# Optimization experiments

Hardware: AMD Instinct MI355X
Metric: run time of the kernel (lower is better)

## Reference

```python
import jax, jax.numpy as jnp
import numpy as np

D_MODEL = 2048
NUM_HEADS = 16
HEAD_DIM = D_MODEL // NUM_HEADS
D_FF = 4 * D_MODEL
B, L = 2, 2048
LN_EPS = 1e-6


def layer_norm(x, scale, bias):
    x32 = x.astype(jnp.float32)
    mu = jnp.mean(x32, axis=-1, keepdims=True)
    var = jnp.mean(jnp.square(x32 - mu), axis=-1, keepdims=True)
    return (x32 - mu) * jax.lax.rsqrt(var + LN_EPS) * scale + bias


def setup_inputs() -> dict:
    key = jax.random.key(0)
    ks = jax.random.split(key, 10)
    s = 1.0 / np.sqrt(D_MODEL)
    x = jax.random.normal(ks[0], (B, L, D_MODEL), dtype=jnp.float32)
    mask = jnp.tril(jnp.ones((L, L), dtype=bool))[None, None, :, :]  # causal [1,1,L,L]
    wq = jax.random.normal(ks[1], (D_MODEL, D_MODEL), jnp.float32) * s
    wk = jax.random.normal(ks[2], (D_MODEL, D_MODEL), jnp.float32) * s
    wv = jax.random.normal(ks[3], (D_MODEL, D_MODEL), jnp.float32) * s
    wo = jax.random.normal(ks[4], (D_MODEL, D_MODEL), jnp.float32) * s
    w1 = jax.random.normal(ks[5], (D_MODEL, D_FF), jnp.float32) * s
    b1 = jnp.zeros((D_FF,), jnp.float32)
    w2 = jax.random.normal(ks[6], (D_FF, D_MODEL), jnp.float32) * (1.0 / np.sqrt(D_FF))
    b2 = jnp.zeros((D_MODEL,), jnp.float32)
    ln1_scale = jnp.ones((D_MODEL,), jnp.float32)
    ln1_bias = jnp.zeros((D_MODEL,), jnp.float32)
    ln2_scale = jnp.ones((D_MODEL,), jnp.float32)
    ln2_bias = jnp.zeros((D_MODEL,), jnp.float32)
    return {"x": x, "mask": mask, "ln1_scale": ln1_scale, "ln1_bias": ln1_bias,
            "wq": wq, "wk": wk, "wv": wv, "wo": wo,
            "ln2_scale": ln2_scale, "ln2_bias": ln2_bias,
            "w1": w1, "b1": b1, "w2": w2, "b2": b2}


def reference(x, mask, ln1_scale, ln1_bias, wq, wk, wv, wo,
              ln2_scale, ln2_bias, w1, b1, w2, b2):
    residual = x
    h = layer_norm(x, ln1_scale, ln1_bias)
    b, l, _ = h.shape
    q = (h @ wq).reshape(b, l, NUM_HEADS, HEAD_DIM)
    k = (h @ wk).reshape(b, l, NUM_HEADS, HEAD_DIM)
    v = (h @ wv).reshape(b, l, NUM_HEADS, HEAD_DIM)
    scores = jnp.einsum('bqhd,bkhd->bhqk', q, k) / jnp.sqrt(jnp.float32(HEAD_DIM))
    scores = jnp.where(mask, scores, -100000.0)
    attn = jax.nn.softmax(scores, axis=-1)
    attn_out = jnp.einsum('bhqk,bkhd->bqhd', attn, v).reshape(b, l, D_MODEL)
    x = residual + attn_out @ wo
    mlp = jax.nn.gelu(layer_norm(x, ln2_scale, ln2_bias) @ w1 + b1)
    return x + mlp @ w2 + b2
```

## Files before the change

### kernel.cpp

```cpp
#include <hip/hip_runtime.h>
#include <hip/hip_bf16.h>

typedef unsigned short u16;
typedef __bf16 bf16x8 __attribute__((ext_vector_type(8)));
typedef float f32x4 __attribute__((ext_vector_type(4)));

#define D_MODEL 2048
#define D_FF    8192
#define NH      16
#define HD      128
#define BATCH   2
#define SEQ     2048
#define ROWS    (BATCH*SEQ)

__device__ __forceinline__ u16 f2bf(float f) {
  union { __hip_bfloat16 h; u16 u; } cv;
  cv.h = __float2bfloat16(f);
  return cv.u;
}

__device__ __forceinline__ void gload16(const u16* g, u16* l) {
  __builtin_amdgcn_global_load_lds((const __attribute__((address_space(1))) void*)g,
                                   (__attribute__((address_space(3))) void*)l,
                                   16, 0, 0);
}

__device__ __forceinline__ float gelu_f(float x) {
  const float k0 = 0.7978845608028654f, k1 = 0.044715f;
  return 0.5f * x * (1.0f + tanhf(k0 * (x + k1 * x * x * x)));
}

__global__ __launch_bounds__(256) void ln_bf16_kernel(
    const float* __restrict__ x, const float* __restrict__ sc,
    const float* __restrict__ bs, u16* __restrict__ out)
{
  __shared__ float red[8];
  const int row = blockIdx.x, t = threadIdx.x;
  const int w = t >> 6, l = t & 63;
  const float* xr = x + (size_t)row * D_MODEL;
  float4 a = ((const float4*)xr)[t*2];
  float4 b = ((const float4*)xr)[t*2+1];
  float s  = a.x+a.y+a.z+a.w + b.x+b.y+b.z+b.w;
  float s2 = a.x*a.x+a.y*a.y+a.z*a.z+a.w*a.w + b.x*b.x+b.y*b.y+b.z*b.z+b.w*b.w;
  for (int off = 32; off; off >>= 1) { s += __shfl_down(s, off); s2 += __shfl_down(s2, off); }
  if (l == 0) { red[w] = s; red[4+w] = s2; }
  __syncthreads();
  s  = red[0]+red[1]+red[2]+red[3];
  s2 = red[4]+red[5]+red[6]+red[7];
  const float mu  = s * (1.0f / D_MODEL);
  const float var = s2 * (1.0f / D_MODEL) - mu * mu;
  const float inv = rsqrtf(var + 1e-6f);
  float4 g0 = ((const float4*)sc)[t*2], g1 = ((const float4*)sc)[t*2+1];
  float4 q0 = ((const float4*)bs)[t*2], q1 = ((const float4*)bs)[t*2+1];
  union { u16 u[8]; uint4 v; } o;
  o.u[0] = f2bf((a.x-mu)*inv*g0.x + q0.x);
  o.u[1] = f2bf((a.y-mu)*inv*g0.y + q0.y);
  o.u[2] = f2bf((a.z-mu)*inv*g0.z + q0.z);
  o.u[3] = f2bf((a.w-mu)*inv*g0.w + q0.w);
  o.u[4] = f2bf((b.x-mu)*inv*g1.x + q1.x);
  o.u[5] = f2bf((b.y-mu)*inv*g1.y + q1.y);
  o.u[6] = f2bf((b.z-mu)*inv*g1.z + q1.z);
  o.u[7] = f2bf((b.w-mu)*inv*g1.w + q1.w);
  *(uint4*)(&out[(size_t)row * D_MODEL + t*8]) = o.v;
}

__global__ __launch_bounds__(256) void transpose_w(
    const float* __restrict__ in, u16* __restrict__ out, int R, int C)
{
  __shared__ float tile[32][33];
  const int t = threadIdx.x;
  const int c0 = blockIdx.x*32, r0 = blockIdx.y*32;
  const int col = t & 31, rb = t >> 5;
#pragma unroll
  for (int i = 0; i < 4; ++i)
    tile[rb + i*8][col] = in[(size_t)(r0 + rb + i*8)*C + c0 + col];
  __syncthreads();
#pragma unroll
  for (int i = 0; i < 4; ++i)
    out[(size_t)(c0 + rb + i*8)*R + r0 + col] = f2bf(tile[col][rb + i*8]);
}

__global__ __launch_bounds__(256) void transpose_v(
    const u16* __restrict__ qkv, u16* __restrict__ vt)
{
  __shared__ u16 tile[32][34];
  const int t = threadIdx.x;
  const int b = blockIdx.z;
  const int c0 = blockIdx.x*32, r0 = blockIdx.y*32;
  const int col = t & 31, rb = t >> 5;
  const u16* inb = qkv + (size_t)b*SEQ*3*D_MODEL + 2*D_MODEL;
#pragma unroll
  for (int i = 0; i < 4; ++i)
    tile[rb+i*8][col] = inb[(size_t)(r0+rb+i*8)*(3*D_MODEL) + c0+col];
  __syncthreads();
  u16* ob = vt + (size_t)b*SEQ*D_MODEL;
#pragma unroll
  for (int i = 0; i < 4; ++i)
    ob[(size_t)(c0+rb+i*8)*SEQ + r0+col] = tile[col][rb+i*8];
}

template<int EPI>
__global__ __launch_bounds__(256, 2) void gemm_p4(
    const u16* __restrict__ A, const u16* __restrict__ BT,
    void* __restrict__ Cout, const float* __restrict__ bias,
    const float* __restrict__ res, int N, int K, int gridN)
{
  __shared__ __align__(16) u16 lds[32768];
  const int t = threadIdx.x;
  const int nwg = gridDim.x;
  const int wg = (int)blockIdx.x;
  const int wgid = (wg & 7) * (nwg >> 3) + (wg >> 3);
  const int bx = wgid % gridN, by = wgid / gridN;
  const int m0 = by * 128, n0 = bx * 128;
  const int w = t >> 6, l = t & 63;
  const int wm = w >> 1, wn = w & 1;
  const int l15 = l & 15, lq = l >> 4;

  const int o0 = t, o1 = 256 + t;
  const int r0 = o0 >> 2, c0s = (o0 & 3) ^ ((r0 >> 1) & 3);
  const int r1 = o1 >> 2, c1s = (o1 & 3) ^ ((r1 >> 1) & 3);
  const u16* a0 = A  + (size_t)(m0 + r0) * K + c0s * 8;
  const u16* a1 = A  + (size_t)(m0 + r1) * K + c1s * 8;
  const u16* b0 = BT + (size_t)(n0 + r0) * K + c0s * 8;
  const u16* b1 = BT + (size_t)(n0 + r1) * K + c1s * 8;

  int offA[4], offB[4];
#pragma unroll
  for (int i = 0; i < 4; ++i) {
    const int ra = wm * 64 + i * 16 + l15;
    offA[i] = ra * 32 + ((lq ^ ((ra >> 1) & 3)) * 8);
    const int rb = wn * 64 + i * 16 + l15;
    offB[i] = 4096 + rb * 32 + ((lq ^ ((rb >> 1) & 3)) * 8);
  }

  f32x4 acc[4][4] = {};
  const int nt = K >> 5;

#define STAGE(tile) { u16* d = &lds[((tile) & 3) * 8192]; \
    gload16(a0 + (size_t)(tile) * 32, d + o0 * 8); \
    gload16(a1 + (size_t)(tile) * 32, d + o1 * 8); \
    gload16(b0 + (size_t)(tile) * 32, d + 4096 + o0 * 8); \
    gload16(b1 + (size_t)(tile) * 32, d + 4096 + o1 * 8); }

#define KSTEP(TT, DOSTAGE, VMSTR) { \
    u16* buf = &lds[((TT) & 3) * 8192]; \
    if (DOSTAGE) STAGE((TT) + 3); \
    bf16x8 af[4], bfr[4]; \
    _Pragma("unroll") \
    for (int i = 0; i < 4; ++i) af[i]  = *(const bf16x8*)&buf[offA[i]]; \
    _Pragma("unroll") \
    for (int i = 0; i < 4; ++i) bfr[i] = *(const bf16x8*)&buf[offB[i]]; \
    __builtin_amdgcn_s_barrier(); \
    asm volatile("s_waitcnt lgkmcnt(0)" ::: "memory"); \
    __builtin_amdgcn_sched_barrier(0); \
    __builtin_amdgcn_s_setprio(1); \
    _Pragma("unroll") \
    for (int mi = 0; mi < 4; ++mi) \
      _Pragma("unroll") \
      for (int ni = 0; ni < 4; ++ni) \
        acc[mi][ni] = __builtin_amdgcn_mfma_f32_16x16x32_bf16(af[mi], bfr[ni], acc[mi][ni], 0, 0, 0); \
    __builtin_amdgcn_s_setprio(0); \
    asm volatile("s_waitcnt " VMSTR ::: "memory"); \
    __builtin_amdgcn_sched_barrier(0); \
    __builtin_amdgcn_s_barrier(); }

  STAGE(0); STAGE(1); STAGE(2);
  asm volatile("s_waitcnt vmcnt(8)" ::: "memory");
  __builtin_amdgcn_sched_barrier(0);
  __builtin_amdgcn_s_barrier();

  for (int tt = 0; tt < nt - 3; ++tt)
    KSTEP(tt, true, "vmcnt(8)")
  KSTEP(nt - 3, false, "vmcnt(4)")
  KSTEP(nt - 2, false, "vmcnt(0)")
  KSTEP(nt - 1, false, "vmcnt(0)")
#undef KSTEP
#undef STAGE

  const int rowb = m0 + wm * 64;
  const int colb = n0 + wn * 64;
#pragma unroll
  for (int mi = 0; mi < 4; ++mi) {
#pragma unroll
    for (int ni = 0; ni < 4; ++ni) {
      const int col = colb + ni * 16 + l15;
      const int row0 = rowb + mi * 16 + lq * 4;
      float bv = (EPI == 2 || EPI == 3) ? bias[col] : 0.f;
#pragma unroll
      for (int r = 0; r < 4; ++r) {
        const float v = acc[mi][ni][r];
        const size_t idx = (size_t)(row0 + r) * N + col;
        if (EPI == 0)      ((u16*)Cout)[idx] = f2bf(v);
        else if (EPI == 1) ((float*)Cout)[idx] = v + res[idx];
        else if (EPI == 2) ((u16*)Cout)[idx] = f2bf(gelu_f(v + bv));
        else               ((float*)Cout)[idx] = v + bv + res[idx];
      }
    }
  }
}

__global__ __launch_bounds__(256) void attn_kernel(
    const u16* __restrict__ qkv, const u16* __restrict__ vt,
    u16* __restrict__ out)
{
  __shared__ u16 Ks[64*128];
  __shared__ u16 Vs[128*64];
  __shared__ u16 Ps[4*16*64];
  const int t = threadIdx.x;
  const int qt = blockIdx.x & 31, bh = blockIdx.x >> 5;
  const int b = bh >> 4, h = bh & 15;
  const int w = t >> 6, l = t & 63;
  const int l15 = l & 15, lq = l >> 4;

  bf16x8 qf[4];
  {
    const u16* qb = qkv + (size_t)(b*SEQ + qt*64 + w*16 + l15)*(3*D_MODEL) + h*HD;
#pragma unroll
    for (int kk = 0; kk < 4; ++kk)
      qf[kk] = *(const bf16x8*)(qb + kk*32 + lq*8);
  }
  float m[4]    = {-INFINITY, -INFINITY, -INFINITY, -INFINITY};
  float lsum[4] = {0.f, 0.f, 0.f, 0.f};
  f32x4 acc_o[8] = {};
  const size_t kbase = (size_t)b*SEQ*(3*D_MODEL) + D_MODEL + h*HD;
  const size_t vbase = (size_t)(b*SEQ + h*HD) * SEQ;
  u16* pw = &Ps[w*1024];

  for (int j = 0; j <= qt; ++j) {
    __syncthreads();
#pragma unroll
    for (int i = 0; i < 4; ++i) {
      const int o16 = i*256 + t;
      {
        const int row = o16 >> 4, cs = o16 & 15;
        const int srcc = cs ^ (row & 7);
        gload16(qkv + kbase + (size_t)(j*64+row)*(3*D_MODEL) + srcc*8, &Ks[o16*8]);
      }
      {
        const int row = o16 >> 3, cs = o16 & 7;
        const int srcc = cs ^ (row & 7);
        gload16(vt + vbase + (size_t)row*SEQ + j*64 + srcc*8, &Vs[o16*8]);
      }
    }
    __syncthreads();

    f32x4 sacc[4] = {};
#pragma unroll
    for (int nf = 0; nf < 4; ++nf) {
      const int kr = nf*16 + l15;
      const int sw = kr & 7;
#pragma unroll
      for (int kk = 0; kk < 4; ++kk) {
        bf16x8 kf = *(const bf16x8*)&Ks[kr*128 + ((kk*4+lq) ^ sw)*8];
        sacc[nf] = __builtin_amdgcn_mfma_f32_16x16x32_bf16(qf[kk], kf, sacc[nf], 0, 0, 0);
      }
    }

    const float scale = 0.08838834764831845f;
    if (j == qt) {
#pragma unroll
      for (int nf = 0; nf < 4; ++nf)
#pragma unroll
        for (int r = 0; r < 4; ++r) {
          float s = sacc[nf][r] * scale;
          const int ki = nf*16 + l15;
          const int qi = w*16 + lq*4 + r;
          if (ki > qi) s = -100000.0f;
          sacc[nf][r] = s;
        }
    } else {
#pragma unroll
      for (int nf = 0; nf < 4; ++nf)
#pragma unroll
        for (int r = 0; r < 4; ++r) sacc[nf][r] *= scale;
    }

    float scal[4];
#pragma unroll
    for (int r = 0; r < 4; ++r) {
      float mx = fmaxf(fmaxf(sacc[0][r], sacc[1][r]), fmaxf(sacc[2][r], sacc[3][r]));
#pragma unroll
      for (int off = 1; off < 16; off <<= 1)
        mx = fmaxf(mx, __shfl_xor(mx, off));
      const float mn = fmaxf(m[r], mx);
      scal[r] = __expf(m[r] - mn);
      m[r] = mn;
      float rs = 0.f;
#pragma unroll
      for (int nf = 0; nf < 4; ++nf) {
        const float p = __expf(sacc[nf][r] - mn);
        sacc[nf][r] = p;
        rs += p;
      }
#pragma unroll
      for (int off = 1; off < 16; off <<= 1)
        rs += __shfl_xor(rs, off);
      lsum[r] = lsum[r]*scal[r] + rs;
    }
#pragma unroll
    for (int nf2 = 0; nf2 < 8; ++nf2)
#pragma unroll
      for (int r = 0; r < 4; ++r) acc_o[nf2][r] *= scal[r];

#pragma unroll
    for (int nf = 0; nf < 4; ++nf)
#pragma unroll
      for (int r = 0; r < 4; ++r) {
        const int qr = lq*4 + r, kc = nf*16 + l15;
        pw[qr*64 + (((kc>>3) ^ (qr&7))*8 + (kc&7))] = f2bf(sacc[nf][r]);
      }

#pragma unroll
    for (int kk2 = 0; kk2 < 2; ++kk2) {
      bf16x8 pf = *(const bf16x8*)&pw[l15*64 + (((kk2*4+lq) ^ (l15&7))*8)];
#pragma unroll
      for (int nf2 = 0; nf2 < 8; ++nf2) {
        const int vr = nf2*16 + l15;
        bf16x8 vf = *(const bf16x8*)&Vs[vr*64 + ((kk2*4+lq) ^ (vr&7))*8];
        acc_o[nf2] = __builtin_amdgcn_mfma_f32_16x16x32_bf16(pf, vf, acc_o[nf2], 0, 0, 0);
      }
    }
  }

  const size_t ro = (size_t)(b*SEQ + qt*64 + w*16 + lq*4);
#pragma unroll
  for (int r = 0; r < 4; ++r) {
    const float inv = 1.0f / lsum[r];
#pragma unroll
    for (int nf2 = 0; nf2 < 8; ++nf2)
      out[(ro + r)*D_MODEL + h*HD + nf2*16 + l15] = f2bf(acc_o[nf2][r] * inv);
  }
}

extern "C" void kernel_launch(void* const* d_in, const int* in_sizes, int n_in,
                              void* d_out, int out_size, void* d_ws, size_t ws_size,
                              hipStream_t stream)
{
  (void)in_sizes; (void)n_in; (void)out_size; (void)ws_size;
  const float* x    = (const float*)d_in[0];
  const float* ln1s = (const float*)d_in[2];
  const float* ln1b = (const float*)d_in[3];
  const float* wq   = (const float*)d_in[4];
  const float* wk   = (const float*)d_in[5];
  const float* wv   = (const float*)d_in[6];
  const float* wo   = (const float*)d_in[7];
  const float* ln2s = (const float*)d_in[8];
  const float* ln2b = (const float*)d_in[9];
  const float* w1   = (const float*)d_in[10];
  const float* b1   = (const float*)d_in[11];
  const float* w2   = (const float*)d_in[12];
  const float* b2   = (const float*)d_in[13];
  float* out = (float*)d_out;

  char* ws = (char*)d_ws;
  constexpr size_t OFF_WQKV = 0;
  constexpr size_t OFF_WO   = OFF_WQKV + (size_t)3*D_MODEL*D_MODEL*2;
  constexpr size_t OFF_W1   = OFF_WO   + (size_t)D_MODEL*D_MODEL*2;
  constexpr size_t OFF_W2   = OFF_W1   + (size_t)D_FF*D_MODEL*2;
  constexpr size_t OFF_H    = OFF_W2   + (size_t)D_MODEL*D_FF*2;
  constexpr size_t OFF_QKV  = OFF_H    + (size_t)ROWS*D_MODEL*2;
  constexpr size_t OFF_VT   = OFF_QKV  + (size_t)ROWS*3*D_MODEL*2;
  constexpr size_t OFF_ATTN = OFF_VT   + (size_t)ROWS*D_MODEL*2;
  constexpr size_t OFF_X2   = OFF_ATTN + (size_t)ROWS*D_MODEL*2;

  u16*   wqkv_bt = (u16*)(ws + OFF_WQKV);
  u16*   wo_bt   = (u16*)(ws + OFF_WO);
  u16*   w1_bt   = (u16*)(ws + OFF_W1);
  u16*   w2_bt   = (u16*)(ws + OFF_W2);
  u16*   h_bf    = (u16*)(ws + OFF_H);
  u16*   qkv     = (u16*)(ws + OFF_QKV);
  u16*   vt      = (u16*)(ws + OFF_VT);
  u16*   act     = qkv;
  u16*   attn    = (u16*)(ws + OFF_ATTN);
  float* x2      = (float*)(ws + OFF_X2);

  const dim3 B256(256);

  transpose_w<<<dim3(64,64),  B256, 0, stream>>>(wq, wqkv_bt,                 D_MODEL, D_MODEL);
  transpose_w<<<dim3(64,64),  B256, 0, stream>>>(wk, wqkv_bt + (size_t)D_MODEL*D_MODEL,   D_MODEL, D_MODEL);
  transpose_w<<<dim3(64,64),  B256, 0, stream>>>(wv, wqkv_bt + (size_t)2*D_MODEL*D_MODEL, D_MODEL, D_MODEL);
  transpose_w<<<dim3(64,64),  B256, 0, stream>>>(wo, wo_bt, D_MODEL, D_MODEL);
  transpose_w<<<dim3(256,64), B256, 0, stream>>>(w1, w1_bt, D_MODEL, D_FF);
  transpose_w<<<dim3(64,256), B256, 0, stream>>>(w2, w2_bt, D_FF, D_MODEL);

  ln_bf16_kernel<<<ROWS, B256, 0, stream>>>(x, ln1s, ln1b, h_bf);
  gemm_p4<0><<<dim3(1536), B256, 0, stream>>>(h_bf, wqkv_bt, qkv, nullptr, nullptr, 3*D_MODEL, D_MODEL, 48);
  transpose_v<<<dim3(64,64,2), B256, 0, stream>>>(qkv, vt);
  attn_kernel<<<dim3(BATCH*NH*32), B256, 0, stream>>>(qkv, vt, attn);
  gemm_p4<1><<<dim3(512), B256, 0, stream>>>(attn, wo_bt, (void*)x2, nullptr, x, D_MODEL, D_MODEL, 16);
  ln_bf16_kernel<<<ROWS, B256, 0, stream>>>(x2, ln2s, ln2b, h_bf);
  gemm_p4<2><<<dim3(2048), B256, 0, stream>>>(h_bf, w1_bt, act, b1, nullptr, D_FF, D_MODEL, 64);
  gemm_p4<3><<<dim3(512), B256, 0, stream>>>(act, w2_bt, (void*)out, b2, x2, D_MODEL, D_FF, 16);
}
```

Before: 772.7 us.

## Add 256x256-tile 8-wave GEMM for QKV and FFN1 projections

Introduces a new GEMM kernel with 512 threads and 256x256 output tiles. It double-buffers K-tiles in 128KB of LDS and splits each K-step into four phases that interleave global-to-LDS loads with MFMA work. QKV and FFN1 GEMMs now use it, to raise arithmetic intensity and cut global/L2 traffic per FLOP. The cost is one workgroup per CU, fewer workgroups (384 and 512) for wave quantization, and heavy register pressure from 128 accumulators. The old kernel's epilogue is simplified to the residual-add path only.

```diff
diff --git a/kernel.cpp b/kernel.cpp
--- a/kernel.cpp
+++ b/kernel.cpp
@@ -100,6 +100,131 @@
 }
 
 template<int EPI>
+__global__ __launch_bounds__(512, 1) void gemm8p(
+    const u16* __restrict__ A, const u16* __restrict__ BT,
+    u16* __restrict__ Cout, const float* __restrict__ bias,
+    int N, int K, int gridN)
+{
+  __shared__ __align__(16) u16 lds[65536];
+  const int t = threadIdx.x;
+  const int nwg = gridDim.x;
+  const int wg = (int)blockIdx.x;
+  const int wgid = (wg & 7) * (nwg >> 3) + (wg >> 3);
+  const int bx = wgid % gridN, by = wgid / gridN;
+  const int m0 = by * 256, n0 = bx * 256;
+  const int w = t >> 6, l = t & 63;
+  const int wm = w >> 2, wn = w & 3;
+  const int l15 = l & 15, lq = l >> 4;
+
+  const int srow = t >> 2;
+  const int c0s  = (t & 3) ^ ((srow >> 1) & 3);
+  const u16* aS0 = A  + (size_t)(m0 + srow) * K + c0s * 8;
+  const u16* aS1 = A  + (size_t)(m0 + 128 + srow) * K + c0s * 8;
+  const u16* bS0 = BT + (size_t)(n0 + srow) * K + c0s * 8;
+  const u16* bS1 = BT + (size_t)(n0 + 128 + srow) * K + c0s * 8;
+
+  int offA_[2][4], offB_[4];
+#pragma unroll
+  for (int mq = 0; mq < 2; ++mq)
+#pragma unroll
+    for (int i2 = 0; i2 < 4; ++i2) {
+      const int ra = wm * 128 + mq * 64 + i2 * 16 + l15;
+      offA_[mq][i2] = ra * 32 + ((lq ^ ((ra >> 1) & 3)) * 8);
+    }
+#pragma unroll
+  for (int j = 0; j < 4; ++j) {
+    const int rb = wn * 64 + j * 16 + l15;
+    offB_[j] = rb * 32 + ((lq ^ ((rb >> 1) & 3)) * 8);
+  }
+
+  f32x4 acc[8][4] = {};
+  bf16x8 bfv[4];
+  const int nt = K >> 6;
+
+#define STAGE_A(dst, Tn, kh) { \
+    gload16(aS0 + (size_t)(Tn)*64 + (kh)*32, (dst) + (kh)*8192 + t*8); \
+    gload16(aS1 + (size_t)(Tn)*64 + (kh)*32, (dst) + (kh)*8192 + 4096 + t*8); }
+#define STAGE_B(dst, Tn, kh) { \
+    gload16(bS0 + (size_t)(Tn)*64 + (kh)*32, (dst) + 16384 + (kh)*8192 + t*8); \
+    gload16(bS1 + (size_t)(Tn)*64 + (kh)*32, (dst) + 16384 + (kh)*8192 + 4096 + t*8); }
+#define VM4 { asm volatile("s_waitcnt vmcnt(4)" ::: "memory"); __builtin_amdgcn_sched_barrier(0); }
+#define VM0 { asm volatile("s_waitcnt vmcnt(0)" ::: "memory"); __builtin_amdgcn_sched_barrier(0); }
+#define NOP { }
+
+#define PHASE(bufc, MQ, KH, DOB, STAGECODE, WAITCODE) { \
+    bf16x8 af_[4]; \
+    _Pragma("unroll") \
+    for (int i2 = 0; i2 < 4; ++i2) \
+      af_[i2] = *(const bf16x8*)&(bufc)[offA_[MQ][i2] + (KH)*8192]; \
+    if (DOB) { \
+      _Pragma("unroll") \
+      for (int j = 0; j < 4; ++j) \
+        bfv[j] = *(const bf16x8*)&(bufc)[offB_[j] + 16384 + (KH)*8192]; \
+    } \
+    STAGECODE; \
+    __builtin_amdgcn_s_barrier(); \
+    asm volatile("s_waitcnt lgkmcnt(0)" ::: "memory"); \
+    __builtin_amdgcn_sched_barrier(0); \
+    __builtin_amdgcn_s_setprio(1); \
+    _Pragma("unroll") \
+    for (int i2 = 0; i2 < 4; ++i2) \
+      _Pragma("unroll") \
+      for (int j = 0; j < 4; ++j) \
+        acc[(MQ)*4 + i2][j] = __builtin_amdgcn_mfma_f32_16x16x32_bf16(af_[i2], bfv[j], acc[(MQ)*4 + i2][j], 0, 0, 0); \
+    __builtin_amdgcn_s_setprio(0); \
+    WAITCODE; \
+    __builtin_amdgcn_s_barrier(); }
+
+  {
+    u16* b0p = lds;
+    STAGE_A(b0p, 0, 0); STAGE_B(b0p, 0, 0); STAGE_A(b0p, 0, 1); STAGE_B(b0p, 0, 1);
+  }
+  VM4;
+  __builtin_amdgcn_s_barrier();
+
+  for (int T = 0; T < nt - 1; ++T) {
+    u16* bufc = &lds[(T & 1) * 32768];
+    u16* bufn = &lds[((T + 1) & 1) * 32768];
+    PHASE(bufc, 0, 0, 1, STAGE_A(bufn, T + 1, 0), NOP);
+    PHASE(bufc, 1, 0, 0, STAGE_B(bufn, T + 1, 0), VM4);
+    PHASE(bufc, 0, 1, 1, STAGE_A(bufn, T + 1, 1), NOP);
+    PHASE(bufc, 1, 1, 0, STAGE_B(bufn, T + 1, 1), VM4);
+  }
+  {
+    u16* bufc = &lds[((nt - 1) & 1) * 32768];
+    PHASE(bufc, 0, 0, 1, NOP, NOP);
+    PHASE(bufc, 1, 0, 0, NOP, VM0);
+    PHASE(bufc, 0, 1, 1, NOP, NOP);
+    PHASE(bufc, 1, 1, 0, NOP, NOP);
+  }
+#undef PHASE
+#undef STAGE_A
+#undef STAGE_B
+#undef VM4
+#undef VM0
+#undef NOP
+
+  const int rowb = m0 + wm * 128;
+  const int colb = n0 + wn * 64;
+#pragma unroll
+  for (int mi = 0; mi < 8; ++mi) {
+#pragma unroll
+    for (int ni = 0; ni < 4; ++ni) {
+      const int col = colb + ni * 16 + l15;
+      const int row0 = rowb + mi * 16 + lq * 4;
+      float bv = (EPI == 2) ? bias[col] : 0.f;
+#pragma unroll
+      for (int r = 0; r < 4; ++r) {
+        const float v = acc[mi][ni][r];
+        const size_t idx = (size_t)(row0 + r) * N + col;
+        if (EPI == 0) Cout[idx] = f2bf(v);
+        else          Cout[idx] = f2bf(gelu_f(v + bv));
+      }
+    }
+  }
+}
+
+template<int EPI>
 __global__ __launch_bounds__(256, 2) void gemm_p4(
     const u16* __restrict__ A, const u16* __restrict__ BT,
     void* __restrict__ Cout, const float* __restrict__ bias,
@@ -185,15 +310,12 @@
     for (int ni = 0; ni < 4; ++ni) {
       const int col = colb + ni * 16 + l15;
       const int row0 = rowb + mi * 16 + lq * 4;
-      float bv = (EPI == 2 || EPI == 3) ? bias[col] : 0.f;
+      float bv = (EPI == 3) ? bias[col] : 0.f;
 #pragma unroll
       for (int r = 0; r < 4; ++r) {
         const float v = acc[mi][ni][r];
         const size_t idx = (size_t)(row0 + r) * N + col;
-        if (EPI == 0)      ((u16*)Cout)[idx] = f2bf(v);
-        else if (EPI == 1) ((float*)Cout)[idx] = v + res[idx];
-        else if (EPI == 2) ((u16*)Cout)[idx] = f2bf(gelu_f(v + bv));
-        else               ((float*)Cout)[idx] = v + bv + res[idx];
+        ((float*)Cout)[idx] = v + bv + ((const float*)res)[idx];
       }
     }
   }
@@ -374,7 +496,7 @@
   u16*   attn    = (u16*)(ws + OFF_ATTN);
   float* x2      = (float*)(ws + OFF_X2);
 
-  const dim3 B256(256);
+  const dim3 B256(256), B512(512);
 
   transpose_w<<<dim3(64,64),  B256, 0, stream>>>(wq, wqkv_bt,                 D_MODEL, D_MODEL);
   transpose_w<<<dim3(64,64),  B256, 0, stream>>>(wk, wqkv_bt + (size_t)D_MODEL*D_MODEL,   D_MODEL, D_MODEL);
@@ -384,11 +506,11 @@
   transpose_w<<<dim3(64,256), B256, 0, stream>>>(w2, w2_bt, D_FF, D_MODEL);
 
   ln_bf16_kernel<<<ROWS, B256, 0, stream>>>(x, ln1s, ln1b, h_bf);
-  gemm_p4<0><<<dim3(1536), B256, 0, stream>>>(h_bf, wqkv_bt, qkv, nullptr, nullptr, 3*D_MODEL, D_MODEL, 48);
+  gemm8p<0><<<dim3(384), B512, 0, stream>>>(h_bf, wqkv_bt, qkv, nullptr, 3*D_MODEL, D_MODEL, 24);
   transpose_v<<<dim3(64,64,2), B256, 0, stream>>>(qkv, vt);
   attn_kernel<<<dim3(BATCH*NH*32), B256, 0, stream>>>(qkv, vt, attn);
   gemm_p4<1><<<dim3(512), B256, 0, stream>>>(attn, wo_bt, (void*)x2, nullptr, x, D_MODEL, D_MODEL, 16);
   ln_bf16_kernel<<<ROWS, B256, 0, stream>>>(x2, ln2s, ln2b, h_bf);
-  gemm_p4<2><<<dim3(2048), B256, 0, stream>>>(h_bf, w1_bt, act, b1, nullptr, D_FF, D_MODEL, 64);
+  gemm8p<2><<<dim3(512), B512, 0, stream>>>(h_bf, w1_bt, act, b1, D_FF, D_MODEL, 32);
   gemm_p4<3><<<dim3(512), B256, 0, stream>>>(act, w2_bt, (void*)out, b2, x2, D_MODEL, D_FF, 16);
 }
```

Result: faster. 743.9 us (-3.7%).

## Use 256-row 8-wave GEMM tiles and pair causal query tiles per attention block

Applied to the files above, without the earlier changes.

Replaces the 128x128 four-wave GEMM with a 512-thread kernel using 256xBNP tiles, a 64-wide K step split into four phases, and double buffering that interleaves staging of the next tile with MFMA work. The larger tiles are meant to raise data reuse per load and cut global traffic. The attention kernel now handles a query tile together with its mirror (qt and 31-qt) in each block, evening out the causal work per block and halving the block count. The GEMMs run one block of 512 threads per CU with a large accumulator array, which raises register pressure and reduces occupancy, and fewer GEMM blocks may leave parts of the machine idle on the smaller GEMMs.

```diff
diff --git a/kernel.cpp b/kernel.cpp
--- a/kernel.cpp
+++ b/kernel.cpp
@@ -99,90 +99,123 @@
     ob[(size_t)(c0+rb+i*8)*SEQ + r0+col] = tile[col][rb+i*8];
 }
 
-template<int EPI>
-__global__ __launch_bounds__(256, 2) void gemm_p4(
+template<int EPI, int BNP>
+__global__ __launch_bounds__(512, 1) void gemm8p(
     const u16* __restrict__ A, const u16* __restrict__ BT,
     void* __restrict__ Cout, const float* __restrict__ bias,
     const float* __restrict__ res, int N, int K, int gridN)
 {
-  __shared__ __align__(16) u16 lds[32768];
+  constexpr int GB    = BNP / 128;
+  constexpr int NI    = BNP / 64;
+  constexpr int BHALF = BNP * 32;
+  constexpr int BUFU  = 16384 + BNP * 64;
+  __shared__ __align__(16) u16 lds[2 * BUFU];
   const int t = threadIdx.x;
   const int nwg = gridDim.x;
   const int wg = (int)blockIdx.x;
   const int wgid = (wg & 7) * (nwg >> 3) + (wg >> 3);
   const int bx = wgid % gridN, by = wgid / gridN;
-  const int m0 = by * 128, n0 = bx * 128;
+  const int m0 = by * 256, n0 = bx * BNP;
   const int w = t >> 6, l = t & 63;
-  const int wm = w >> 1, wn = w & 1;
+  const int wm = w >> 2, wn = w & 3;
   const int l15 = l & 15, lq = l >> 4;
 
-  const int o0 = t, o1 = 256 + t;
-  const int r0 = o0 >> 2, c0s = (o0 & 3) ^ ((r0 >> 1) & 3);
-  const int r1 = o1 >> 2, c1s = (o1 & 3) ^ ((r1 >> 1) & 3);
-  const u16* a0 = A  + (size_t)(m0 + r0) * K + c0s * 8;
-  const u16* a1 = A  + (size_t)(m0 + r1) * K + c1s * 8;
-  const u16* b0 = BT + (size_t)(n0 + r0) * K + c0s * 8;
-  const u16* b1 = BT + (size_t)(n0 + r1) * K + c1s * 8;
-
-  int offA[4], offB[4];
-#pragma unroll
-  for (int i = 0; i < 4; ++i) {
-    const int ra = wm * 64 + i * 16 + l15;
-    offA[i] = ra * 32 + ((lq ^ ((ra >> 1) & 3)) * 8);
-    const int rb = wn * 64 + i * 16 + l15;
-    offB[i] = 4096 + rb * 32 + ((lq ^ ((rb >> 1) & 3)) * 8);
-  }
-
-  f32x4 acc[4][4] = {};
-  const int nt = K >> 5;
-
-#define STAGE(tile) { u16* d = &lds[((tile) & 3) * 8192]; \
-    gload16(a0 + (size_t)(tile) * 32, d + o0 * 8); \
-    gload16(a1 + (size_t)(tile) * 32, d + o1 * 8); \
-    gload16(b0 + (size_t)(tile) * 32, d + 4096 + o0 * 8); \
-    gload16(b1 + (size_t)(tile) * 32, d + 4096 + o1 * 8); }
-
-#define KSTEP(TT, DOSTAGE, VMSTR) { \
-    u16* buf = &lds[((TT) & 3) * 8192]; \
-    if (DOSTAGE) STAGE((TT) + 3); \
-    bf16x8 af[4], bfr[4]; \
+  const int srow = t >> 2;
+  const int c0s  = (t & 3) ^ ((srow >> 1) & 3);
+  const u16* aS0 = A  + (size_t)(m0 + srow) * K + c0s * 8;
+  const u16* aS1 = A  + (size_t)(m0 + 128 + srow) * K + c0s * 8;
+  const u16* bS0 = BT + (size_t)(n0 + srow) * K + c0s * 8;
+  const u16* bS1 = BT + (size_t)(n0 + (GB == 2 ? 128 : 0) + srow) * K + c0s * 8;
+
+  int offA_[2][4], offB_[NI];
+#pragma unroll
+  for (int mq = 0; mq < 2; ++mq)
+#pragma unroll
+    for (int i2 = 0; i2 < 4; ++i2) {
+      const int ra = wm * 128 + mq * 64 + i2 * 16 + l15;
+      offA_[mq][i2] = ra * 32 + ((lq ^ ((ra >> 1) & 3)) * 8);
+    }
+#pragma unroll
+  for (int j = 0; j < NI; ++j) {
+    const int rb = wn * (BNP / 4) + j * 16 + l15;
+    offB_[j] = rb * 32 + ((lq ^ ((rb >> 1) & 3)) * 8);
+  }
+
+  f32x4 acc[8][NI] = {};
+  bf16x8 bfv[NI];
+  const int nt = K >> 6;
+
+#define STAGE_A(dst, Tn, kh) { \
+    gload16(aS0 + (size_t)(Tn)*64 + (kh)*32, (dst) + (kh)*8192 + t*8); \
+    gload16(aS1 + (size_t)(Tn)*64 + (kh)*32, (dst) + (kh)*8192 + 4096 + t*8); }
+#define STAGE_B(dst, Tn, kh) { \
+    gload16(bS0 + (size_t)(Tn)*64 + (kh)*32, (dst) + 16384 + (kh)*BHALF + t*8); \
+    if (GB == 2) gload16(bS1 + (size_t)(Tn)*64 + (kh)*32, (dst) + 16384 + (kh)*BHALF + 4096 + t*8); }
+#define VMS { if (GB == 2) { asm volatile("s_waitcnt vmcnt(4)" ::: "memory"); } \
+              else        { asm volatile("s_waitcnt vmcnt(3)" ::: "memory"); } \
+              __builtin_amdgcn_sched_barrier(0); }
+#define VM0 { asm volatile("s_waitcnt vmcnt(0)" ::: "memory"); __builtin_amdgcn_sched_barrier(0); }
+#define NOP { }
+
+#define PHASE(bufc, MQ, KH, DOB, STAGECODE, WAITCODE) { \
+    bf16x8 af_[4]; \
     _Pragma("unroll") \
-    for (int i = 0; i < 4; ++i) af[i]  = *(const bf16x8*)&buf[offA[i]]; \
-    _Pragma("unroll") \
-    for (int i = 0; i < 4; ++i) bfr[i] = *(const bf16x8*)&buf[offB[i]]; \
+    for (int i2 = 0; i2 < 4; ++i2) \
+      af_[i2] = *(const bf16x8*)&(bufc)[offA_[MQ][i2] + (KH)*8192]; \
+    if (DOB) { \
+      _Pragma("unroll") \
+      for (int j = 0; j < NI; ++j) \
+        bfv[j] = *(const bf16x8*)&(bufc)[offB_[j] + 16384 + (KH)*BHALF]; \
+    } \
+    STAGECODE; \
     __builtin_amdgcn_s_barrier(); \
     asm volatile("s_waitcnt lgkmcnt(0)" ::: "memory"); \
     __builtin_amdgcn_sched_barrier(0); \
     __builtin_amdgcn_s_setprio(1); \
     _Pragma("unroll") \
-    for (int mi = 0; mi < 4; ++mi) \
+    for (int i2 = 0; i2 < 4; ++i2) \
       _Pragma("unroll") \
-      for (int ni = 0; ni < 4; ++ni) \
-        acc[mi][ni] = __builtin_amdgcn_mfma_f32_16x16x32_bf16(af[mi], bfr[ni], acc[mi][ni], 0, 0, 0); \
+      for (int j = 0; j < NI; ++j) \
+        acc[(MQ)*4 + i2][j] = __builtin_amdgcn_mfma_f32_16x16x32_bf16(af_[i2], bfv[j], acc[(MQ)*4 + i2][j], 0, 0, 0); \
     __builtin_amdgcn_s_setprio(0); \
-    asm volatile("s_waitcnt " VMSTR ::: "memory"); \
-    __builtin_amdgcn_sched_barrier(0); \
+    WAITCODE; \
     __builtin_amdgcn_s_barrier(); }
 
-  STAGE(0); STAGE(1); STAGE(2);
-  asm volatile("s_waitcnt vmcnt(8)" ::: "memory");
-  __builtin_amdgcn_sched_barrier(0);
+  {
+    u16* b0p = lds;
+    STAGE_A(b0p, 0, 0); STAGE_B(b0p, 0, 0); STAGE_A(b0p, 0, 1); STAGE_B(b0p, 0, 1);
+  }
+  VMS;
   __builtin_amdgcn_s_barrier();
 
-  for (int tt = 0; tt < nt - 3; ++tt)
-    KSTEP(tt, true, "vmcnt(8)")
-  KSTEP(nt - 3, false, "vmcnt(4)")
-  KSTEP(nt - 2, false, "vmcnt(0)")
-  KSTEP(nt - 1, false, "vmcnt(0)")
-#undef KSTEP
-#undef STAGE
-
-  const int rowb = m0 + wm * 64;
-  const int colb = n0 + wn * 64;
-#pragma unroll
-  for (int mi = 0; mi < 4; ++mi) {
-#pragma unroll
-    for (int ni = 0; ni < 4; ++ni) {
+  for (int T = 0; T < nt - 1; ++T) {
+    u16* bufc = &lds[(T & 1) * BUFU];
+    u16* bufn = &lds[((T + 1) & 1) * BUFU];
+    PHASE(bufc, 0, 0, 1, STAGE_A(bufn, T + 1, 0), NOP);
+    PHASE(bufc, 1, 0, 0, STAGE_B(bufn, T + 1, 0), VMS);
+    PHASE(bufc, 0, 1, 1, STAGE_A(bufn, T + 1, 1), NOP);
+    PHASE(bufc, 1, 1, 0, STAGE_B(bufn, T + 1, 1), VMS);
+  }
+  {
+    u16* bufc = &lds[((nt - 1) & 1) * BUFU];
+    PHASE(bufc, 0, 0, 1, NOP, NOP);
+    PHASE(bufc, 1, 0, 0, NOP, VM0);
+    PHASE(bufc, 0, 1, 1, NOP, NOP);
+    PHASE(bufc, 1, 1, 0, NOP, NOP);
+  }
+#undef PHASE
+#undef STAGE_A
+#undef STAGE_B
+#undef VMS
+#undef VM0
+#undef NOP
+
+  const int rowb = m0 + wm * 128;
+  const int colb = n0 + wn * (BNP / 4);
+#pragma unroll
+  for (int mi = 0; mi < 8; ++mi) {
+#pragma unroll
+    for (int ni = 0; ni < NI; ++ni) {
       const int col = colb + ni * 16 + l15;
       const int row0 = rowb + mi * 16 + lq * 4;
       float bv = (EPI == 2 || EPI == 3) ? bias[col] : 0.f;
@@ -207,128 +240,133 @@
   __shared__ u16 Vs[128*64];
   __shared__ u16 Ps[4*16*64];
   const int t = threadIdx.x;
-  const int qt = blockIdx.x & 31, bh = blockIdx.x >> 5;
+  const int pairi = blockIdx.x & 15, bh = blockIdx.x >> 4;
   const int b = bh >> 4, h = bh & 15;
   const int w = t >> 6, l = t & 63;
   const int l15 = l & 15, lq = l >> 4;
-
-  bf16x8 qf[4];
-  {
-    const u16* qb = qkv + (size_t)(b*SEQ + qt*64 + w*16 + l15)*(3*D_MODEL) + h*HD;
-#pragma unroll
-    for (int kk = 0; kk < 4; ++kk)
-      qf[kk] = *(const bf16x8*)(qb + kk*32 + lq*8);
-  }
-  float m[4]    = {-INFINITY, -INFINITY, -INFINITY, -INFINITY};
-  float lsum[4] = {0.f, 0.f, 0.f, 0.f};
-  f32x4 acc_o[8] = {};
   const size_t kbase = (size_t)b*SEQ*(3*D_MODEL) + D_MODEL + h*HD;
   const size_t vbase = (size_t)(b*SEQ + h*HD) * SEQ;
   u16* pw = &Ps[w*1024];
 
-  for (int j = 0; j <= qt; ++j) {
-    __syncthreads();
-#pragma unroll
-    for (int i = 0; i < 4; ++i) {
-      const int o16 = i*256 + t;
-      {
-        const int row = o16 >> 4, cs = o16 & 15;
-        const int srcc = cs ^ (row & 7);
-        gload16(qkv + kbase + (size_t)(j*64+row)*(3*D_MODEL) + srcc*8, &Ks[o16*8]);
-      }
-      {
-        const int row = o16 >> 3, cs = o16 & 7;
-        const int srcc = cs ^ (row & 7);
-        gload16(vt + vbase + (size_t)row*SEQ + j*64 + srcc*8, &Vs[o16*8]);
-      }
+  for (int qsel = 0; qsel < 2; ++qsel) {
+    const int qt = qsel ? (31 - pairi) : pairi;
+
+    bf16x8 qf[4];
+    {
+      const u16* qb = qkv + (size_t)(b*SEQ + qt*64 + w*16 + l15)*(3*D_MODEL) + h*HD;
+#pragma unroll
+      for (int kk = 0; kk < 4; ++kk)
+        qf[kk] = *(const bf16x8*)(qb + kk*32 + lq*8);
+    }
+    float m[4]    = {-INFINITY, -INFINITY, -INFINITY, -INFINITY};
+    float lsum[4] = {0.f, 0.f, 0.f, 0.f};
+    f32x4 acc_o[8] = {};
+
+    for (int j = 0; j <= qt; ++j) {
+      __syncthreads();
+#pragma unroll
+      for (int i = 0; i < 4; ++i) {
+        const int o16 = i*256 + t;
+        {
+          const int row = o16 >> 4, cs = o16 & 15;
+          const int srcc = cs ^ (row & 7);
+          gload16(qkv + kbase + (size_t)(j*64+row)*(3*D_MODEL) + srcc*8, &Ks[o16*8]);
+        }
+        {
+          const int row = o16 >> 3, cs = o16 & 7;
+          const int srcc = cs ^ (row & 7);
+          gload16(vt + vbase + (size_t)row*SEQ + j*64 + srcc*8, &Vs[o16*8]);
+        }
+      }
+      __syncthreads();
+
+      f32x4 sacc[4] = {};
+#pragma unroll
+      for (int nf = 0; nf < 4; ++nf) {
+        const int kr = nf*16 + l15;
+        const int sw = kr & 7;
+#pragma unroll
+        for (int kk = 0; kk < 4; ++kk) {
+          bf16x8 kf = *(const bf16x8*)&Ks[kr*128 + ((kk*4+lq) ^ sw)*8];
+          sacc[nf] = __builtin_amdgcn_mfma_f32_16x16x32_bf16(qf[kk], kf, sacc[nf], 0, 0, 0);
+        }
+      }
+
+      const float scale = 0.08838834764831845f;
+      if (j == qt) {
+#pragma unroll
+        for (int nf = 0; nf < 4; ++nf)
+#pragma unroll
+          for (int r = 0; r < 4; ++r) {
+            float s = sacc[nf][r] * scale;
+            const int ki = nf*16 + l15;
+            const int qi = w*16 + lq*4 + r;
+            if (ki > qi) s = -100000.0f;
+            sacc[nf][r] = s;
+          }
+      } else {
+#pragma unroll
+        for (int nf = 0; nf < 4; ++nf)
+#pragma unroll
+          for (int r = 0; r < 4; ++r) sacc[nf][r] *= scale;
+      }
+
+      float scal[4];
+#pragma unroll
+      for (int r = 0; r < 4; ++r) {
+        float mx = fmaxf(fmaxf(sacc[0][r], sacc[1][r]), fmaxf(sacc[2][r], sacc[3][r]));
+#pragma unroll
+        for (int off = 1; off < 16; off <<= 1)
+          mx = fmaxf(mx, __shfl_xor(mx, off));
+        const float mn = fmaxf(m[r], mx);
+        scal[r] = __expf(m[r] - mn);
+        m[r] = mn;
+        float rs = 0.f;
+#pragma unroll
+        for (int nf = 0; nf < 4; ++nf) {
+          const float p = __expf(sacc[nf][r] - mn);
+          sacc[nf][r] = p;
+          rs += p;
+        }
+#pragma unroll
+        for (int off = 1; off < 16; off <<= 1)
+          rs += __shfl_xor(rs, off);
+        lsum[r] = lsum[r]*scal[r] + rs;
+      }
+#pragma unroll
+      for (int nf2 = 0; nf2 < 8; ++nf2)
+#pragma unroll
+        for (int r = 0; r < 4; ++r) acc_o[nf2][r] *= scal[r];
+
+#pragma unroll
+      for (int nf = 0; nf < 4; ++nf)
+#pragma unroll
+        for (int r = 0; r < 4; ++r) {
+          const int qr = lq*4 + r, kc = nf*16 + l15;
+          pw[qr*64 + (((kc>>3) ^ (qr&7))*8 + (kc&7))] = f2bf(sacc[nf][r]);
+        }
+
+#pragma unroll
+      for (int kk2 = 0; kk2 < 2; ++kk2) {
+        bf16x8 pf = *(const bf16x8*)&pw[l15*64 + (((kk2*4+lq) ^ (l15&7))*8)];
+#pragma unroll
+        for (int nf2 = 0; nf2 < 8; ++nf2) {
+          const int vr = nf2*16 + l15;
+          bf16x8 vf = *(const bf16x8*)&Vs[vr*64 + ((kk2*4+lq) ^ (vr&7))*8];
+          acc_o[nf2] = __builtin_amdgcn_mfma_f32_16x16x32_bf16(pf, vf, acc_o[nf2], 0, 0, 0);
+        }
+      }
+    }
+
+    const size_t ro = (size_t)(b*SEQ + qt*64 + w*16 + lq*4);
+#pragma unroll
+    for (int r = 0; r < 4; ++r) {
+      const float inv = 1.0f / lsum[r];
+#pragma unroll
+      for (int nf2 = 0; nf2 < 8; ++nf2)
+        out[(ro + r)*D_MODEL + h*HD + nf2*16 + l15] = f2bf(acc_o[nf2][r] * inv);
     }
     __syncthreads();
-
-    f32x4 sacc[4] = {};
-#pragma unroll
-    for (int nf = 0; nf < 4; ++nf) {
-      const int kr = nf*16 + l15;
-      const int sw = kr & 7;
-#pragma unroll
-      for (int kk = 0; kk < 4; ++kk) {
-        bf16x8 kf = *(const bf16x8*)&Ks[kr*128 + ((kk*4+lq) ^ sw)*8];
-        sacc[nf] = __builtin_amdgcn_mfma_f32_16x16x32_bf16(qf[kk], kf, sacc[nf], 0, 0, 0);
-      }
-    }
-
-    const float scale = 0.08838834764831845f;
-    if (j == qt) {
-#pragma unroll
-      for (int nf = 0; nf < 4; ++nf)
-#pragma unroll
-        for (int r = 0; r < 4; ++r) {
-          float s = sacc[nf][r] * scale;
-          const int ki = nf*16 + l15;
-          const int qi = w*16 + lq*4 + r;
-          if (ki > qi) s = -100000.0f;
-          sacc[nf][r] = s;
-        }
-    } else {
-#pragma unroll
-      for (int nf = 0; nf < 4; ++nf)
-#pragma unroll
-        for (int r = 0; r < 4; ++r) sacc[nf][r] *= scale;
-    }
-
-    float scal[4];
-#pragma unroll
-    for (int r = 0; r < 4; ++r) {
-      float mx = fmaxf(fmaxf(sacc[0][r], sacc[1][r]), fmaxf(sacc[2][r], sacc[3][r]));
-#pragma unroll
-      for (int off = 1; off < 16; off <<= 1)
-        mx = fmaxf(mx, __shfl_xor(mx, off));
-      const float mn = fmaxf(m[r], mx);
-      scal[r] = __expf(m[r] - mn);
-      m[r] = mn;
-      float rs = 0.f;
-#pragma unroll
-      for (int nf = 0; nf < 4; ++nf) {
-        const float p = __expf(sacc[nf][r] - mn);
-        sacc[nf][r] = p;
-        rs += p;
-      }
-#pragma unroll
-      for (int off = 1; off < 16; off <<= 1)
-        rs += __shfl_xor(rs, off);
-      lsum[r] = lsum[r]*scal[r] + rs;
-    }
-#pragma unroll
-    for (int nf2 = 0; nf2 < 8; ++nf2)
-#pragma unroll
-      for (int r = 0; r < 4; ++r) acc_o[nf2][r] *= scal[r];
-
-#pragma unroll
-    for (int nf = 0; nf < 4; ++nf)
-#pragma unroll
-      for (int r = 0; r < 4; ++r) {
-        const int qr = lq*4 + r, kc = nf*16 + l15;
-        pw[qr*64 + (((kc>>3) ^ (qr&7))*8 + (kc&7))] = f2bf(sacc[nf][r]);
-      }
-
-#pragma unroll
-    for (int kk2 = 0; kk2 < 2; ++kk2) {
-      bf16x8 pf = *(const bf16x8*)&pw[l15*64 + (((kk2*4+lq) ^ (l15&7))*8)];
-#pragma unroll
-      for (int nf2 = 0; nf2 < 8; ++nf2) {
-        const int vr = nf2*16 + l15;
-        bf16x8 vf = *(const bf16x8*)&Vs[vr*64 + ((kk2*4+lq) ^ (vr&7))*8];
-        acc_o[nf2] = __builtin_amdgcn_mfma_f32_16x16x32_bf16(pf, vf, acc_o[nf2], 0, 0, 0);
-      }
-    }
-  }
-
-  const size_t ro = (size_t)(b*SEQ + qt*64 + w*16 + lq*4);
-#pragma unroll
-  for (int r = 0; r < 4; ++r) {
-    const float inv = 1.0f / lsum[r];
-#pragma unroll
-    for (int nf2 = 0; nf2 < 8; ++nf2)
-      out[(ro + r)*D_MODEL + h*HD + nf2*16 + l15] = f2bf(acc_o[nf2][r] * inv);
   }
 }
 
@@ -374,7 +412,7 @@
   u16*   attn    = (u16*)(ws + OFF_ATTN);
   float* x2      = (float*)(ws + OFF_X2);
 
-  const dim3 B256(256);
+  const dim3 B256(256), B512(512);
 
   transpose_w<<<dim3(64,64),  B256, 0, stream>>>(wq, wqkv_bt,                 D_MODEL, D_MODEL);
   transpose_w<<<dim3(64,64),  B256, 0, stream>>>(wk, wqkv_bt + (size_t)D_MODEL*D_MODEL,   D_MODEL, D_MODEL);
@@ -384,11 +422,11 @@
   transpose_w<<<dim3(64,256), B256, 0, stream>>>(w2, w2_bt, D_FF, D_MODEL);
 
   ln_bf16_kernel<<<ROWS, B256, 0, stream>>>(x, ln1s, ln1b, h_bf);
-  gemm_p4<0><<<dim3(1536), B256, 0, stream>>>(h_bf, wqkv_bt, qkv, nullptr, nullptr, 3*D_MODEL, D_MODEL, 48);
+  gemm8p<0,128><<<dim3(768), B512, 0, stream>>>(h_bf, wqkv_bt, qkv, nullptr, nullptr, 3*D_MODEL, D_MODEL, 48);
   transpose_v<<<dim3(64,64,2), B256, 0, stream>>>(qkv, vt);
-  attn_kernel<<<dim3(BATCH*NH*32), B256, 0, stream>>>(qkv, vt, attn);
-  gemm_p4<1><<<dim3(512), B256, 0, stream>>>(attn, wo_bt, (void*)x2, nullptr, x, D_MODEL, D_MODEL, 16);
+  attn_kernel<<<dim3(BATCH*NH*16), B256, 0, stream>>>(qkv, vt, attn);
+  gemm8p<1,128><<<dim3(256), B512, 0, stream>>>(attn, wo_bt, (void*)x2, nullptr, x, D_MODEL, D_MODEL, 16);
   ln_bf16_kernel<<<ROWS, B256, 0, stream>>>(x2, ln2s, ln2b, h_bf);
-  gemm_p4<2><<<dim3(2048), B256, 0, stream>>>(h_bf, w1_bt, act, b1, nullptr, D_FF, D_MODEL, 64);
-  gemm_p4<3><<<dim3(512), B256, 0, stream>>>(act, w2_bt, (void*)out, b2, x2, D_MODEL, D_FF, 16);
-}
+  gemm8p<2,256><<<dim3(512), B512, 0, stream>>>(h_bf, w1_bt, act, b1, nullptr, D_FF, D_MODEL, 32);
+  gemm8p<3,128><<<dim3(256), B512, 0, stream>>>(act, w2_bt, (void*)out, b2, x2, D_MODEL, D_FF, 16);
+}
```

After: 668.4 us. 1.16x faster.
